# Optimization experiments

Measured on AMD Instinct MI355X. Metric: run time of the kernel, lower is better.

The kernel has to match this reference:

```python
import jax, jax.numpy as jnp
from jax import lax
import numpy as np

EPS = 1e-5

def _bn(x, g, b, m, v):
    # inference-mode BatchNorm2d over channel dim (NCHW)
    scale = (g * lax.rsqrt(v + EPS))[None, :, None, None]
    return (x - m[None, :, None, None]) * scale + b[None, :, None, None]

def _conv(x, w, dil, pad):
    return lax.conv_general_dilated(
        x, w, window_strides=(1, 1), padding=[(pad, pad), (pad, pad)],
        rhs_dilation=(dil, dil), dimension_numbers=('NCHW', 'OIHW', 'NCHW'))

def _interleave(b0, b1, b2, b3):
    # out[2i+r, 2j+c] = branch[2r+c][i, j]  (equivalent to the mask*nearest-upsample trick)
    bs, C, H, W = b0.shape
    row0 = jnp.stack([b0, b1], axis=-1)          # (bs,C,H,W,2) -> c
    row1 = jnp.stack([b2, b3], axis=-1)
    s = jnp.stack([row0, row1], axis=-2)          # (bs,C,H,W,2,2) -> (...,r,c)
    return s.transpose(0, 1, 2, 4, 3, 5).reshape(bs, C, 2 * H, 2 * W)

def setup_inputs() -> dict:
    key = jax.random.key(0)
    ks = iter(jax.random.split(key, 40))
    B, Cin, Cout, H = 8, 256, 128, 64
    inp = {"x": jax.random.normal(next(ks), (B, Cin, H, H), jnp.float32)}
    inp["w0"] = jax.random.normal(next(ks), (Cout, Cin, 1, 1), jnp.float32) * 0.05
    for i in (1, 2, 3):
        inp[f"w{i}"] = jax.random.normal(next(ks), (Cout, Cin, 3, 3), jnp.float32) * 0.02
    inp["wp"] = jax.random.normal(next(ks), (Cout, Cout, 1, 1), jnp.float32) * 0.05
    for t in ("0", "1", "2", "3", "p"):
        inp[f"g{t}"] = 1.0 + 0.1 * jax.random.normal(next(ks), (Cout,), jnp.float32)
        inp[f"b{t}"] = 0.1 * jax.random.normal(next(ks), (Cout,), jnp.float32)
        inp[f"m{t}"] = 0.05 * jax.random.normal(next(ks), (Cout,), jnp.float32)
        inp[f"v{t}"] = jax.random.uniform(next(ks), (Cout,), jnp.float32, 0.5, 1.5)
    return inp

def reference(x, w0, w1, w2, w3, wp,
              g0, b0, m0, v0, g1, b1, m1, v1,
              g2, b2, m2, v2, g3, b3, m3, v3,
              gp, bp, mp, vp):
    RATES = (6, 12, 18)
    br0 = jax.nn.relu(_bn(_conv(x, w0, 1, 0), g0, b0, m0, v0))
    br1 = jax.nn.relu(_bn(_conv(x, w1, RATES[0], RATES[0]), g1, b1, m1, v1))
    br2 = jax.nn.relu(_bn(_conv(x, w2, RATES[1], RATES[1]), g2, b2, m2, v2))
    br3 = jax.nn.relu(_bn(_conv(x, w3, RATES[2], RATES[2]), g3, b3, m3, v3))
    up = _interleave(br0, br1, br2, br3)          # (B, Cout, 2H, 2W)
    return jax.nn.relu(_bn(_conv(up, wp, 1, 0), gp, bp, mp, vp))  # dropout: eval identity
```

## Files before the change

### kernel.cpp

```cpp
#include <hip/hip_runtime.h>
#include <stdint.h>

typedef unsigned int uint32;
typedef uint16_t u16;
typedef short short8 __attribute__((ext_vector_type(8)));
typedef short shortx4 __attribute__((ext_vector_type(4)));
typedef float floatx4 __attribute__((ext_vector_type(4)));

#define BN_EPS 1e-5f

#define XROW 25600
#define XPLANE 1638400
#define XB_SHORTS 13107200
#define ZROW_SHORTS 25600

#define OFF0 0
#define OFF1 32768
#define OFF2 327680
#define OFF3 622592
#define OFFP 917504
#define WPK_SHORTS 933888
#define U_B0 4096
#define U_B  36864
#define U_TOT 116736

__device__ __forceinline__ u16 f2bf(float f) {
  uint32 u = __float_as_uint(f);
  u += 0x7fffu + ((u >> 16) & 1u);
  return (u16)(u >> 16);
}

__global__ void k_xcvt(const float* __restrict__ x, u16* __restrict__ xb) {
  int bid = blockIdx.x, tid = threadIdx.x;
  if (bid == 512) {
    uint32* z = (uint32*)(xb + XB_SHORTS);
    #pragma unroll
    for (int r = 0; r < 50; ++r) z[r * 256 + tid] = 0;
    return;
  }
  int n = bid >> 6, i = bid & 63;
  uint32* rw = (uint32*)(xb + (size_t)n * XPLANE + (size_t)i * XROW);
  #pragma unroll
  for (int e = 0; e < 18; ++e) {
    int idx = e * 256 + tid;
    int colid = idx >> 7;
    int jp = (colid < 18) ? colid : (colid + 64);
    rw[jp * 128 + (idx & 127)] = 0;
  }
  int ci2 = tid & 127, jh = tid >> 7;
  const float* xs = x + ((size_t)(n * 256 + 2 * ci2) * 64 + i) * 64 + jh * 32;
  #pragma unroll 4
  for (int j = 0; j < 32; ++j) {
    float f0 = xs[j];
    float f1 = xs[4096 + j];
    uint32 pk = (uint32)f2bf(f0) | ((uint32)f2bf(f1) << 16);
    rw[(jh * 32 + j + 18) * 128 + ci2] = pk;
  }
}

__global__ void k_wpack(const float* __restrict__ w0, const float* __restrict__ w1,
                        const float* __restrict__ w2, const float* __restrict__ w3,
                        const float* __restrict__ wp, u16* __restrict__ wpk) {
  int g = blockIdx.x * 256 + threadIdx.x;
  if (g >= U_TOT) return;
  const float* w; int Cin, t, q, u, off; bool k3;
  if (g < U_B0) {
    int blk = g >> 10; w = w0; Cin = 256; k3 = false; t = 0; q = blk; u = g & 1023;
    off = OFF0 + blk * 8192;
  } else if (g < U_B0 + U_B) {
    int g1 = g - U_B0; int blk = g1 >> 10; w = w1; Cin = 256; k3 = true;
    t = blk >> 2; q = blk & 3; u = g1 & 1023; off = OFF1 + blk * 8192;
  } else if (g < U_B0 + 2*U_B) {
    int g1 = g - (U_B0 + U_B); int blk = g1 >> 10; w = w2; Cin = 256; k3 = true;
    t = blk >> 2; q = blk & 3; u = g1 & 1023; off = OFF2 + blk * 8192;
  } else if (g < U_B0 + 3*U_B) {
    int g1 = g - (U_B0 + 2*U_B); int blk = g1 >> 10; w = w3; Cin = 256; k3 = true;
    t = blk >> 2; q = blk & 3; u = g1 & 1023; off = OFF3 + blk * 8192;
  } else {
    int g1 = g - (U_B0 + 3*U_B); int blk = g1 >> 10; w = wp; Cin = 128; k3 = false;
    t = 0; q = blk; u = g1 & 1023; off = OFFP + blk * 8192;
  }
  int slot = u >> 7, co = u & 127;
  int ci0 = q * 64 + slot * 8;
  int kh = k3 ? (t / 3) : 0, kw = k3 ? (t % 3) : 0;
  union { short8 s; u16 us[8]; } v;
  #pragma unroll
  for (int e = 0; e < 8; ++e) {
    int ci = ci0 + e;
    float wv = k3 ? w[((co * Cin + ci) * 3 + kh) * 3 + kw] : w[co * Cin + ci];
    v.us[e] = f2bf(wv);
  }
  *(short8*)(wpk + off + u * 8) = v.s;
}

__global__ void k_bn(const float* g0,const float* b0,const float* m0,const float* v0,
                     const float* g1,const float* b1,const float* m1,const float* v1,
                     const float* g2,const float* b2,const float* m2,const float* v2,
                     const float* g3,const float* b3,const float* m3,const float* v3,
                     const float* gp,const float* bp,const float* mp,const float* vp,
                     float* __restrict__ bn) {
  int i = blockIdx.x * 256 + threadIdx.x;
  if (i >= 640) return;
  int t = i >> 7, co = i & 127;
  const float *G, *B, *M, *V;
  if      (t == 0) { G=g0; B=b0; M=m0; V=v0; }
  else if (t == 1) { G=g1; B=b1; M=m1; V=v1; }
  else if (t == 2) { G=g2; B=b2; M=m2; V=v2; }
  else if (t == 3) { G=g3; B=b3; M=m3; V=v3; }
  else             { G=gp; B=bp; M=mp; V=vp; }
  float s = G[co] * rsqrtf(V[co] + BN_EPS);
  bn[t * 256 + co]       = s;
  bn[t * 256 + 128 + co] = B[co] - M[co] * s;
}

__global__ __launch_bounds__(256, 3)
void k_main(const u16* __restrict__ xb, const u16* __restrict__ wpk,
            const float* __restrict__ bn, float* __restrict__ out) {
  __shared__ __align__(16) u16 BP[16384];

  int tid = threadIdx.x;
  int bid = blockIdx.x;
  int n = bid & 7;
  int rest = bid >> 3;
  int tile = rest >> 2;
  int b = (rest ^ (rest >> 5)) & 3;
  int i0 = tile * 2;
  int lane = tid & 63, wid = tid >> 6;
  int wm = wid >> 1, wn = wid & 1;
  int m16 = lane & 15, hh = lane >> 4;

  const u16* xg = xb + (size_t)n * XPLANE;
  const u16* zr = xb + XB_SHORTS;
  int d = (b == 0) ? 0 : ((b == 1) ? 6 : ((b == 2) ? 12 : 18));
  int NS = ((b == 0) ? 1 : 9) * 4;
  int woff8 = ((b == 0) ? OFF0 : (b == 1) ? OFF1 : (b == 2) ? OFF2 : OFF3) / 8;

  const short8* wpk8 = (const short8*)wpk;
  short8* BsS8 = (short8*)BP;
  const short8* PsS8 = (const short8*)BP;

  floatx4 acc[4][4];
  #pragma unroll
  for (int a1 = 0; a1 < 4; ++a1)
    #pragma unroll
    for (int a2 = 0; a2 < 4; ++a2) acc[a1][a2] = (floatx4){0.f, 0.f, 0.f, 0.f};

  short8 rb[4];
  int cg = tid & 7, pxo = tid >> 3;
  int arow = wm * 64 + m16;

  auto prefetchB = [&](int s) {
    int t = s >> 2, q = s & 3;
    int di = d * (t / 3 - 1);
    int dj = d * (t % 3 - 1);
    #pragma unroll
    for (int k = 0; k < 4; ++k) {
      int px = k * 32 + pxo;
      int ii = i0 + (k >> 1) + di;
      const u16* base = (ii >= 0 && ii < 64) ? (xg + ii * XROW) : zr;
      int jj = (px & 63) + 18 + dj;
      rb[k] = *(const short8*)(base + jj * 256 + q * 64 + cg * 8);
    }
  };

  prefetchB(0);

  for (int s = 0; s < NS; ++s) {
    __builtin_amdgcn_s_barrier();
    #pragma unroll
    for (int k = 0; k < 4; ++k) {
      int px = k * 32 + pxo;
      BsS8[px * 8 + (cg ^ (px & 7))] = rb[k];
    }
    short8 af[2][4];
    {
      int abase = woff8 + s * 1024;
      #pragma unroll
      for (int kk = 0; kk < 2; ++kk)
        #pragma unroll
        for (int f = 0; f < 4; ++f)
          af[kk][f] = wpk8[abase + (kk * 4 + hh) * 128 + arow + f * 16];
    }
    if (s + 1 < NS) prefetchB(s + 1);
    asm volatile("s_waitcnt lgkmcnt(0)" ::: "memory");
    __builtin_amdgcn_s_barrier();
    #pragma unroll
    for (int kk = 0; kk < 2; ++kk) {
      short8 bfr[4];
      #pragma unroll
      for (int f = 0; f < 4; ++f) {
        int px = wn * 64 + f * 16 + m16;
        bfr[f] = BsS8[px * 8 + ((kk * 4 + hh) ^ (px & 7))];
      }
      #pragma unroll
      for (int fm = 0; fm < 4; ++fm)
        #pragma unroll
        for (int fn = 0; fn < 4; ++fn)
          acc[fm][fn] = __builtin_amdgcn_mfma_f32_16x16x32_bf16(
              af[kk][fm], bfr[fn], acc[fm][fn], 0, 0, 0);
    }
  }

  __syncthreads();
  #pragma unroll
  for (int fm = 0; fm < 4; ++fm) {
    int co_base = wm * 64 + fm * 16 + hh * 4;
    float sc[4], sh[4];
    #pragma unroll
    for (int r = 0; r < 4; ++r) {
      sc[r] = bn[b * 256 + co_base + r];
      sh[r] = bn[b * 256 + 128 + co_base + r];
    }
    #pragma unroll
    for (int fn = 0; fn < 4; ++fn) {
      int px = wn * 64 + fn * 16 + m16;
      int sw = (px >> 1) & 7;
      int slot = (co_base >> 3) ^ sw;
      union { shortx4 s4; u16 us[4]; } pk;
      #pragma unroll
      for (int r = 0; r < 4; ++r)
        pk.us[r] = f2bf(fmaxf(acc[fm][fn][r] * sc[r] + sh[r], 0.f));
      *(shortx4*)&BP[px * 128 + slot * 8 + (co_base & 7)] = pk.s4;
    }
  }

  floatx4 acc2[4][4];
  #pragma unroll
  for (int a1 = 0; a1 < 4; ++a1)
    #pragma unroll
    for (int a2 = 0; a2 < 4; ++a2) acc2[a1][a2] = (floatx4){0.f, 0.f, 0.f, 0.f};

  __syncthreads();
  #pragma unroll
  for (int q = 0; q < 2; ++q) {
    #pragma unroll
    for (int kk = 0; kk < 2; ++kk) {
      short8 af2[4], bfr[4];
      #pragma unroll
      for (int f = 0; f < 4; ++f)
        af2[f] = wpk8[OFFP / 8 + q * 1024 + (kk * 4 + hh) * 128 + arow + f * 16];
      #pragma unroll
      for (int f = 0; f < 4; ++f) {
        int px = wn * 64 + f * 16 + m16;
        int slot = q * 8 + kk * 4 + hh;
        bfr[f] = PsS8[px * 16 + (slot ^ ((px >> 1) & 7))];
      }
      #pragma unroll
      for (int fm = 0; fm < 4; ++fm)
        #pragma unroll
        for (int fn = 0; fn < 4; ++fn)
          acc2[fm][fn] = __builtin_amdgcn_mfma_f32_16x16x32_bf16(
              af2[fm], bfr[fn], acc2[fm][fn], 0, 0, 0);
    }
  }

  int rb2 = b >> 1, cb = b & 1;
  #pragma unroll
  for (int fm = 0; fm < 4; ++fm) {
    #pragma unroll
    for (int r = 0; r < 4; ++r) {
      int co = wm * 64 + fm * 16 + hh * 4 + r;
      float s  = bn[1024 + co];
      float sh = bn[1024 + 128 + co];
      #pragma unroll
      for (int fn = 0; fn < 4; ++fn) {
        int px = wn * 64 + fn * 16 + m16;
        int i = i0 + (px >> 6), j = px & 63;
        float v = fmaxf(acc2[fm][fn][r] * s + sh, 0.f);
        out[(((n * 128 + co) * 128) + (2 * i + rb2)) * 128 + (2 * j + cb)] = v;
      }
    }
  }
}

extern "C" void kernel_launch(void* const* d_in, const int* in_sizes, int n_in,
                              void* d_out, int out_size, void* d_ws, size_t ws_size,
                              hipStream_t stream) {
  const float* x  = (const float*)d_in[0];
  const float* w0 = (const float*)d_in[1];
  const float* w1 = (const float*)d_in[2];
  const float* w2 = (const float*)d_in[3];
  const float* w3 = (const float*)d_in[4];
  const float* wp = (const float*)d_in[5];

  u16* xbuf = (u16*)d_ws;
  u16* wpk  = (u16*)d_ws + (XB_SHORTS + ZROW_SHORTS);
  float* bn = (float*)((char*)d_ws + (size_t)(XB_SHORTS + ZROW_SHORTS + WPK_SHORTS) * 2);

  k_xcvt<<<513, 256, 0, stream>>>(x, xbuf);
  k_wpack<<<456, 256, 0, stream>>>(w0, w1, w2, w3, wp, wpk);
  k_bn<<<3, 256, 0, stream>>>(
      (const float*)d_in[6],  (const float*)d_in[7],  (const float*)d_in[8],  (const float*)d_in[9],
      (const float*)d_in[10], (const float*)d_in[11], (const float*)d_in[12], (const float*)d_in[13],
      (const float*)d_in[14], (const float*)d_in[15], (const float*)d_in[16], (const float*)d_in[17],
      (const float*)d_in[18], (const float*)d_in[19], (const float*)d_in[20], (const float*)d_in[21],
      (const float*)d_in[22], (const float*)d_in[23], (const float*)d_in[24], (const float*)d_in[25],
      bn);
  k_main<<<1024, 256, 0, stream>>>(xbuf, wpk, bn, (float*)d_out);
}
```

Measured before the change: 104.3 us.

## Load conv operands directly into registers with double-buffered prefetch, drop LDS staging

The main conv loop no longer stages the input tile through shared memory with two barriers per step. Each wave now loads its own A and B MFMA fragments straight from global memory into two register buffers, prefetching step s+1 while computing step s, and raises wave priority around the MFMA bursts. The projection weights are also loaded before the barrier. This removes LDS round-trips and barrier stalls, but doubles register use (occupancy hint lowered from 3 to 2 blocks) and issues redundant global loads, since both wm waves load the same B and both wn waves load the same A.

```diff
diff --git a/kernel.cpp b/kernel.cpp
--- a/kernel.cpp
+++ b/kernel.cpp
@@ -113,7 +113,40 @@
   bn[t * 256 + 128 + co] = B[co] - M[co] * s;
 }
 
-__global__ __launch_bounds__(256, 3)
+#define PREFETCH(sv, AF, BF) do {                                              \
+    int t_ = (sv) >> 2, q_ = (sv) & 3;                                         \
+    int di_ = d * (t_ / 3 - 1);                                                \
+    int dj_ = d * (t_ % 3 - 1);                                                \
+    int abase_ = woff8 + (sv) * 1024;                                          \
+    _Pragma("unroll")                                                          \
+    for (int kk_ = 0; kk_ < 2; ++kk_)                                          \
+      _Pragma("unroll")                                                        \
+      for (int f_ = 0; f_ < 4; ++f_)                                           \
+        AF[kk_][f_] = wpk8[abase_ + (kk_ * 4 + hh) * 128 + arow + f_ * 16];    \
+    int ii_ = i0 + wn + di_;                                                   \
+    const u16* base_ = (ii_ >= 0 && ii_ < 64) ? (xg + ii_ * XROW) : zr;        \
+    _Pragma("unroll")                                                          \
+    for (int kk_ = 0; kk_ < 2; ++kk_)                                          \
+      _Pragma("unroll")                                                        \
+      for (int f_ = 0; f_ < 4; ++f_)                                           \
+        BF[kk_][f_] = *(const short8*)(base_ + (f_ * 16 + m16 + 18 + dj_) * 256\
+                                       + q_ * 64 + kk_ * 32 + hh * 8);         \
+  } while (0)
+
+#define CONSUME(AF, BF) do {                                                   \
+    __builtin_amdgcn_s_setprio(1);                                             \
+    _Pragma("unroll")                                                          \
+    for (int kk_ = 0; kk_ < 2; ++kk_)                                          \
+      _Pragma("unroll")                                                        \
+      for (int fm_ = 0; fm_ < 4; ++fm_)                                        \
+        _Pragma("unroll")                                                      \
+        for (int fn_ = 0; fn_ < 4; ++fn_)                                      \
+          acc[fm_][fn_] = __builtin_amdgcn_mfma_f32_16x16x32_bf16(             \
+              AF[kk_][fm_], BF[kk_][fn_], acc[fm_][fn_], 0, 0, 0);             \
+    __builtin_amdgcn_s_setprio(0);                                             \
+  } while (0)
+
+__global__ __launch_bounds__(256, 2)
 void k_main(const u16* __restrict__ xb, const u16* __restrict__ wpk,
             const float* __restrict__ bn, float* __restrict__ out) {
   __shared__ __align__(16) u16 BP[16384];
@@ -136,8 +169,8 @@
   int woff8 = ((b == 0) ? OFF0 : (b == 1) ? OFF1 : (b == 2) ? OFF2 : OFF3) / 8;
 
   const short8* wpk8 = (const short8*)wpk;
-  short8* BsS8 = (short8*)BP;
   const short8* PsS8 = (const short8*)BP;
+  int arow = wm * 64 + m16;
 
   floatx4 acc[4][4];
   #pragma unroll
@@ -145,63 +178,16 @@
     #pragma unroll
     for (int a2 = 0; a2 < 4; ++a2) acc[a1][a2] = (floatx4){0.f, 0.f, 0.f, 0.f};
 
-  short8 rb[4];
-  int cg = tid & 7, pxo = tid >> 3;
-  int arow = wm * 64 + m16;
-
-  auto prefetchB = [&](int s) {
-    int t = s >> 2, q = s & 3;
-    int di = d * (t / 3 - 1);
-    int dj = d * (t % 3 - 1);
-    #pragma unroll
-    for (int k = 0; k < 4; ++k) {
-      int px = k * 32 + pxo;
-      int ii = i0 + (k >> 1) + di;
-      const u16* base = (ii >= 0 && ii < 64) ? (xg + ii * XROW) : zr;
-      int jj = (px & 63) + 18 + dj;
-      rb[k] = *(const short8*)(base + jj * 256 + q * 64 + cg * 8);
-    }
-  };
-
-  prefetchB(0);
-
-  for (int s = 0; s < NS; ++s) {
-    __builtin_amdgcn_s_barrier();
-    #pragma unroll
-    for (int k = 0; k < 4; ++k) {
-      int px = k * 32 + pxo;
-      BsS8[px * 8 + (cg ^ (px & 7))] = rb[k];
-    }
-    short8 af[2][4];
-    {
-      int abase = woff8 + s * 1024;
-      #pragma unroll
-      for (int kk = 0; kk < 2; ++kk)
-        #pragma unroll
-        for (int f = 0; f < 4; ++f)
-          af[kk][f] = wpk8[abase + (kk * 4 + hh) * 128 + arow + f * 16];
-    }
-    if (s + 1 < NS) prefetchB(s + 1);
-    asm volatile("s_waitcnt lgkmcnt(0)" ::: "memory");
-    __builtin_amdgcn_s_barrier();
-    #pragma unroll
-    for (int kk = 0; kk < 2; ++kk) {
-      short8 bfr[4];
-      #pragma unroll
-      for (int f = 0; f < 4; ++f) {
-        int px = wn * 64 + f * 16 + m16;
-        bfr[f] = BsS8[px * 8 + ((kk * 4 + hh) ^ (px & 7))];
-      }
-      #pragma unroll
-      for (int fm = 0; fm < 4; ++fm)
-        #pragma unroll
-        for (int fn = 0; fn < 4; ++fn)
-          acc[fm][fn] = __builtin_amdgcn_mfma_f32_16x16x32_bf16(
-              af[kk][fm], bfr[fn], acc[fm][fn], 0, 0, 0);
-    }
-  }
-
-  __syncthreads();
+  short8 a0[2][4], b0[2][4], a1r[2][4], b1r[2][4];
+
+  PREFETCH(0, a0, b0);
+  for (int s = 0; s < NS; s += 2) {
+    PREFETCH(s + 1, a1r, b1r);
+    CONSUME(a0, b0);
+    if (s + 2 < NS) PREFETCH(s + 2, a0, b0);
+    CONSUME(a1r, b1r);
+  }
+
   #pragma unroll
   for (int fm = 0; fm < 4; ++fm) {
     int co_base = wm * 64 + fm * 16 + hh * 4;
@@ -224,21 +210,28 @@
     }
   }
 
+  short8 af2[2][2][4];
+  #pragma unroll
+  for (int q = 0; q < 2; ++q)
+    #pragma unroll
+    for (int kk = 0; kk < 2; ++kk)
+      #pragma unroll
+      for (int f = 0; f < 4; ++f)
+        af2[q][kk][f] = wpk8[OFFP / 8 + q * 1024 + (kk * 4 + hh) * 128 + arow + f * 16];
+
+  __syncthreads();
+
   floatx4 acc2[4][4];
   #pragma unroll
   for (int a1 = 0; a1 < 4; ++a1)
     #pragma unroll
     for (int a2 = 0; a2 < 4; ++a2) acc2[a1][a2] = (floatx4){0.f, 0.f, 0.f, 0.f};
 
-  __syncthreads();
   #pragma unroll
   for (int q = 0; q < 2; ++q) {
     #pragma unroll
     for (int kk = 0; kk < 2; ++kk) {
-      short8 af2[4], bfr[4];
-      #pragma unroll
-      for (int f = 0; f < 4; ++f)
-        af2[f] = wpk8[OFFP / 8 + q * 1024 + (kk * 4 + hh) * 128 + arow + f * 16];
+      short8 bfr[4];
       #pragma unroll
       for (int f = 0; f < 4; ++f) {
         int px = wn * 64 + f * 16 + m16;
@@ -250,7 +243,7 @@
         #pragma unroll
         for (int fn = 0; fn < 4; ++fn)
           acc2[fm][fn] = __builtin_amdgcn_mfma_f32_16x16x32_bf16(
-              af2[fm], bfr[fn], acc2[fm][fn], 0, 0, 0);
+              af2[q][kk][fm], bfr[fn], acc2[fm][fn], 0, 0, 0);
     }
   }
 
```

Measured after the change: 183.0 us. +75.5%, slower.
